# Kernel tuning notes

Hardware: AMD Instinct MI355X
Metric: run time of the kernel (lower is better)

Reference implementation:

```python
import jax, jax.numpy as jnp
import numpy as np

N_NODES = 40000
N_EDGES = 640000
N_GRAPHS = 64
F_IN = 32       # fourier_order*4
D_EMB = 256     # int(0.5*512)
D_HID = 512     # int(0.5*1024)
D_FC = 1024     # int(0.5*2048)
N_CLS = 10


def setup_inputs() -> dict:
    key = jax.random.key(0)
    ks = iter(jax.random.split(key, 40))
    rn = lambda shape, s=0.05: jax.random.normal(next(ks), shape, jnp.float32) * s
    inp = {
        'x': jax.random.normal(next(ks), (N_NODES, F_IN), jnp.float32),
        'edge_index': jax.random.randint(next(ks), (2, N_EDGES), 0, N_NODES, jnp.int32),
        'edge_attr': jax.random.uniform(next(ks), (N_EDGES, 1), jnp.float32),
        'batch': jnp.sort(jax.random.randint(next(ks), (N_NODES,), 0, N_GRAPHS, jnp.int32)),
        # embedding MLP
        'emb_w1': rn((F_IN, D_EMB)), 'emb_b1': jnp.zeros((D_EMB,), jnp.float32),
        'emb_w2': rn((D_EMB, D_EMB)), 'emb_b2': jnp.zeros((D_EMB,), jnp.float32),
        # edge_proj MLP
        'ep_w1': rn((1, 64)), 'ep_b1': jnp.zeros((64,), jnp.float32),
        'ep_w2': rn((64, 1)), 'ep_b2': jnp.zeros((1,), jnp.float32),
        # GCNConv weights (x @ W + b, PyG convention)
        'w_c1': rn((D_EMB, D_HID)), 'b_c1': jnp.zeros((D_HID,), jnp.float32),
        'w_c2': rn((D_HID, D_HID)), 'b_c2': jnp.zeros((D_HID,), jnp.float32),
        'w_c3': rn((D_HID, D_HID)), 'b_c3': jnp.zeros((D_HID,), jnp.float32),
        'w_c4': rn((D_HID, D_HID)), 'b_c4': jnp.zeros((D_HID,), jnp.float32),
        'w_c5': rn((D_HID, D_HID)), 'b_c5': jnp.zeros((D_HID,), jnp.float32),
        'w_c6': rn((D_HID, D_HID)), 'b_c6': jnp.zeros((D_HID,), jnp.float32),
        # head
        'fc1_w': rn((D_HID, D_FC)), 'fc1_b': jnp.zeros((D_FC,), jnp.float32),
        'head_w': rn((D_FC, N_CLS)), 'head_b': jnp.zeros((N_CLS,), jnp.float32),
    }
    return inp


def _gcn_conv(x, src, dst, norm, W, b):
    # PyG GCNConv: linear transform, then normalized scatter-add aggregation, then bias
    h = x @ W                                   # [N, d_out]
    msg = h[src] * norm[:, None]                # [E+N, d_out] gathered messages
    agg = jax.ops.segment_sum(msg, dst, num_segments=N_NODES)
    return agg + b


def _forward(x, edge_attr, emb_w1, emb_b1, emb_w2, emb_b2, ep_w1, ep_b1, ep_w2, ep_b2,
             w_c1, b_c1, w_c2, b_c2, w_c3, b_c3, w_c4, b_c4, w_c5, b_c5, w_c6, b_c6,
             fc1_w, fc1_b, head_w, head_b, edge_index, batch):
    # edge weights from edge_proj MLP (sigmoid output in (0,1))
    ew = jax.nn.sigmoid(jax.nn.relu(edge_attr @ ep_w1 + ep_b1) @ ep_w2 + ep_b2)[:, 0]  # [E]
    # gcn_norm with self loops (identical for every conv layer -> compute once)
    loops = jnp.arange(N_NODES, dtype=edge_index.dtype)
    src = jnp.concatenate([edge_index[0], loops])
    dst = jnp.concatenate([edge_index[1], loops])
    w = jnp.concatenate([ew, jnp.ones((N_NODES,), ew.dtype)])
    deg = jax.ops.segment_sum(w, dst, num_segments=N_NODES)
    dinv = jnp.where(deg > 0, jax.lax.rsqrt(jnp.maximum(deg, 1e-12)), 0.0)
    norm = dinv[src] * w * dinv[dst]            # [E+N]

    h = jax.nn.relu(jax.nn.relu(x @ emb_w1 + emb_b1) @ emb_w2 + emb_b2)
    h = _gcn_conv(h, src, dst, norm, w_c1, b_c1)
    skip = jax.nn.relu(h)
    h = _gcn_conv(skip, src, dst, norm, w_c2, b_c2)
    h = jax.nn.relu(h)
    h = _gcn_conv(h, src, dst, norm, w_c3, b_c3)
    skip = jax.nn.relu(h) + skip                # has_skip=True
    h = _gcn_conv(skip, src, dst, norm, w_c4, b_c4)  # is_deep=True
    h = jax.nn.relu(h)
    h = _gcn_conv(h, src, dst, norm, w_c5, b_c5)
    h = jax.nn.relu(h)
    h = _gcn_conv(h, src, dst, norm, w_c6, b_c6)
    skip = jax.nn.relu(h) + skip

    # global mean pool over graphs
    sums = jax.ops.segment_sum(skip, batch, num_segments=N_GRAPHS)
    cnts = jax.ops.segment_sum(jnp.ones((N_NODES,), skip.dtype), batch, num_segments=N_GRAPHS)
    pooled = sums / jnp.maximum(cnts, 1.0)[:, None]   # [G, D_HID]

    out = jax.nn.relu(pooled @ fc1_w + fc1_b) @ head_w + head_b   # [G, N_CLS]
    return out


def reference(x, edge_index, edge_attr, batch, emb_w1, emb_b1, emb_w2, emb_b2,
              ep_w1, ep_b1, ep_w2, ep_b2, w_c1, b_c1, w_c2, b_c2, w_c3, b_c3,
              w_c4, b_c4, w_c5, b_c5, w_c6, b_c6, fc1_w, fc1_b, head_w, head_b):
    return _forward(x, edge_attr, emb_w1, emb_b1, emb_w2, emb_b2, ep_w1, ep_b1, ep_w2, ep_b2,
                    w_c1, b_c1, w_c2, b_c2, w_c3, b_c3, w_c4, b_c4, w_c5, b_c5, w_c6, b_c6,
                    fc1_w, fc1_b, head_w, head_b, edge_index, batch)
```

## Files before the change

### kernel.cpp

```cpp
#include <hip/hip_runtime.h>
#include <math.h>

#define N_NODES 40000
#define MP      40192
#define NROWB   157
#define N_EDGES 640000
#define N_GRAPHS 64
#define F_IN 32
#define D_EMB 256
#define D_HID 512
#define D_FC 1024
#define N_CLS 10

typedef _Float16 f16x8 __attribute__((ext_vector_type(8)));
typedef float f32x4  __attribute__((ext_vector_type(4)));
typedef unsigned short u16;

template <int N> struct VecU;
template <> struct VecU<2> { typedef unsigned T __attribute__((ext_vector_type(2))); };
template <> struct VecU<4> { typedef unsigned T __attribute__((ext_vector_type(4))); };

__device__ __forceinline__ float h2f(u16 u) {
    union { u16 s; _Float16 h; } v; v.s = u; return (float)v.h;
}
__device__ __forceinline__ u16 f2h(float f) {
    union { u16 s; _Float16 h; } v; v.h = (_Float16)f; return v.s;
}
__device__ __forceinline__ void async16(void* lds, const void* g) {
    __builtin_amdgcn_global_load_lds((const __attribute__((address_space(1))) void*)g,
                                     (__attribute__((address_space(3))) void*)lds, 16, 0, 0);
}

__device__ __forceinline__ int pk_idx(int r, int q) {
    int rp = r >> 1;
    int g  = (((r & 1) << 2) | q) ^ (rp & 7);
    return rp * 64 + g * 8;
}

__global__ void prep_all(const float* __restrict__ x, u16* __restrict__ xb, u16* __restrict__ G,
                         float* __restrict__ deg, int* __restrict__ cnt, int* __restrict__ cursor,
                         float* __restrict__ sums) {
    int i = blockIdx.x * blockDim.x + threadIdx.x;
    if (i < N_NODES) { deg[i] = 1.0f; cnt[i] = 0; cursor[i] = 0; }
    if (i < MP * F_IN) {
        int row = i >> 5, colk = i & 31;
        float v = (row < N_NODES) ? x[i] : 0.f;
        size_t idx = (size_t)(row >> 8) * 8192 + pk_idx(row & 255, colk >> 3) + (colk & 7);
        xb[idx] = f2h(v);
    }
    if (i < 16 * 3072) {
        int kc = i / 3072, rem = i % 3072;
        G[(size_t)(156 * 16 + kc) * 8192 + 5120 + rem] = 0;
    } else if (i < 16 * 3072 + 8 * 3072) {
        int j = i - 16 * 3072;
        int kc = j / 3072, rem = j % 3072;
        G[(size_t)(156 * 8 + kc) * 8192 + 5120 + rem] = 0;
    }
    if (i < N_GRAPHS * D_HID) sums[i] = 0.f;
}

__global__ void edge_mlp_deg(const float* __restrict__ edge_attr,
                             const float* __restrict__ ep_w1, const float* __restrict__ ep_b1,
                             const float* __restrict__ ep_w2, const float* __restrict__ ep_b2,
                             const int* __restrict__ dst,
                             float* __restrict__ ew, float* __restrict__ deg, int* __restrict__ cnt) {
    __shared__ float w1[64], b1[64], w2[64];
    int t = threadIdx.x;
    if (t < 64) { w1[t] = ep_w1[t]; b1[t] = ep_b1[t]; w2[t] = ep_w2[t]; }
    __syncthreads();
    int e = blockIdx.x * blockDim.x + t;
    if (e >= N_EDGES) return;
    float x = edge_attr[e];
    float s = ep_b2[0];
#pragma unroll
    for (int j = 0; j < 64; ++j) s += fmaxf(x * w1[j] + b1[j], 0.f) * w2[j];
    float sig = 1.f / (1.f + expf(-s));
    ew[e] = sig;
    int d = dst[e];
    atomicAdd(&deg[d], sig);
    atomicAdd(&cnt[d], 1);
}

__global__ void dinv_kernel(const float* __restrict__ deg, float* __restrict__ dinv,
                            float* __restrict__ nloop) {
    int i = blockIdx.x * blockDim.x + threadIdx.x;
    if (i >= N_NODES) return;
    float d = deg[i];
    float r = (d > 0.f) ? rsqrtf(fmaxf(d, 1e-12f)) : 0.f;
    dinv[i] = r;
    nloop[i] = r * r;
}

__global__ void scan_kernel(const int* __restrict__ cnt, int* __restrict__ rowptr) {
    __shared__ int part[1024];
    int t = threadIdx.x;
    const int PER = (N_NODES + 1023) / 1024;
    int base = t * PER;
    int s = 0;
    for (int k = 0; k < PER; ++k) { int i = base + k; if (i < N_NODES) s += cnt[i]; }
    part[t] = s;
    __syncthreads();
    for (int off = 1; off < 1024; off <<= 1) {
        int v = (t >= off) ? part[t - off] : 0;
        __syncthreads();
        part[t] += v;
        __syncthreads();
    }
    int run = (t == 0) ? 0 : part[t - 1];
    for (int k = 0; k < PER; ++k) {
        int i = base + k;
        if (i < N_NODES) { rowptr[i] = run; run += cnt[i]; }
    }
    if (t == 1023) rowptr[N_NODES] = run;
}

__global__ void fill_csr_kernel(const int* __restrict__ src, const int* __restrict__ dst,
                                const float* __restrict__ ew, const float* __restrict__ dinv,
                                const int* __restrict__ rowptr, int* __restrict__ cursor,
                                int2* __restrict__ cv) {
    int e = blockIdx.x * blockDim.x + threadIdx.x;
    if (e >= N_EDGES) return;
    int d = dst[e];
    int s = src[e];
    float n = dinv[s] * ew[e] * dinv[d];
    int p = rowptr[d] + atomicAdd(&cursor[d], 1);
    cv[p] = make_int2(s, __float_as_int(n));
}

struct WPair { const float* s; u16* d; int K; int N; };
struct WP8 { WPair m[8]; };

__global__ void wprep_all(WP8 a) {
    __shared__ u16 th[32][33];
    WPair w = a.m[blockIdx.z];
    int n0 = blockIdx.x * 32;
    int k0 = blockIdx.y * 32;
    if (n0 >= w.N || k0 >= w.K) return;
    int tx = threadIdx.x, ty = threadIdx.y;
#pragma unroll
    for (int r = 0; r < 4; ++r) {
        int k = ty + r * 8;
        th[k][tx] = f2h(w.s[(size_t)(k0 + k) * w.N + n0 + tx]);
    }
    __syncthreads();
#pragma unroll
    for (int r = 0; r < 4; ++r) {
        int n = ty + r * 8;
        int R = n0 + n;
        int kcol = k0 + tx;
        size_t idx = ((size_t)(R >> 7) * (w.K >> 5) + (kcol >> 5)) * 4096
                   + pk_idx(R & 127, (kcol >> 3) & 3) + (kcol & 7);
        w.d[idx] = th[tx][n];
    }
}

__launch_bounds__(512)
__global__ void mfma_gemm(const u16* __restrict__ A,
                          const u16* __restrict__ W,
                          const float* __restrict__ bias,
                          const u16* __restrict__ skip,
                          u16* __restrict__ C, u16* __restrict__ Cpk,
                          int K, int N,
                          const int* __restrict__ batch, float* __restrict__ pool) {
    __shared__ __align__(16) u16 Wl[32768];
    __shared__ int sbatch[128];

    const int nColB = N >> 6;
    int b = blockIdx.x;
    int rowI = (b >> 3) / nColB * 8 + (b & 7);
    int colI = (b >> 3) % nColB;
    if (rowI >= NROWB) return;
    int rowBase = rowI * 256;
    int colBase = colI * 64;

    int t = threadIdx.x;
    int lane = t & 63;
    int wave = t >> 6;
    int quad = lane >> 4;
    int mrow = lane & 15;
    int nIter = K >> 5;

    int sw = (((mrow & 1) << 2) | quad) ^ ((mrow >> 1) & 7);
    int laneA = (wave * 16 + (mrow >> 1)) * 64 + sw * 8;
    int laneW = (mrow >> 1) * 64 + sw * 8;

    const u16* pA = A + (size_t)rowI * nIter * 8192;

    f16x8 aA0 = *(const f16x8*)&pA[laneA];
    f16x8 aA1 = *(const f16x8*)&pA[laneA + 512];
    f16x8 aB0, aB1;

    {
        const u16* ws = W + ((size_t)(colI >> 1) * nIter) * 4096 + (colI & 1) * 2048;
        for (int kc = wave; kc < nIter; kc += 8) {
            const u16* s = ws + (size_t)kc * 4096;
            u16* d = &Wl[kc * 2048];
            async16(&d[0],    s + lane * 8);
            async16(&d[512],  s + 512 + lane * 8);
            async16(&d[1024], s + 1024 + lane * 8);
            async16(&d[1536], s + 1536 + lane * 8);
        }
    }
    asm volatile("s_waitcnt vmcnt(0)" ::: "memory");
    __syncthreads();

    f32x4 acc[2][4] = {};

    for (int it = 0; it < nIter; it += 2) {
        if (it + 1 < nIter) {
            const u16* nA = pA + (size_t)(it + 1) * 8192;
            aB0 = *(const f16x8*)&nA[laneA];
            aB1 = *(const f16x8*)&nA[laneA + 512];
        }
        __builtin_amdgcn_sched_barrier(0);
        {
            const u16* Wc = &Wl[it * 2048];
#pragma unroll
            for (int j = 0; j < 4; ++j) {
                f16x8 w = *(const f16x8*)&Wc[laneW + j * 512];
                acc[0][j] = __builtin_amdgcn_mfma_f32_16x16x32_f16(aA0, w, acc[0][j], 0, 0, 0);
                acc[1][j] = __builtin_amdgcn_mfma_f32_16x16x32_f16(aA1, w, acc[1][j], 0, 0, 0);
            }
        }
        if (it + 1 < nIter) {
            if (it + 2 < nIter) {
                const u16* nA = pA + (size_t)(it + 2) * 8192;
                aA0 = *(const f16x8*)&nA[laneA];
                aA1 = *(const f16x8*)&nA[laneA + 512];
            }
            __builtin_amdgcn_sched_barrier(0);
            const u16* Wc = &Wl[(it + 1) * 2048];
#pragma unroll
            for (int j = 0; j < 4; ++j) {
                f16x8 w = *(const f16x8*)&Wc[laneW + j * 512];
                acc[0][j] = __builtin_amdgcn_mfma_f32_16x16x32_f16(aB0, w, acc[0][j], 0, 0, 0);
                acc[1][j] = __builtin_amdgcn_mfma_f32_16x16x32_f16(aB1, w, acc[1][j], 0, 0, 0);
            }
        }
    }
    __syncthreads();

    u16* eb = Wl;
    const int ES = 72;
#pragma unroll
    for (int ph = 0; ph < 2; ++ph) {
        if ((wave >> 2) == ph) {
#pragma unroll
            for (int j = 0; j < 4; ++j) {
                int col = colBase + j * 16 + mrow;
                float bv = bias[col];
#pragma unroll
                for (int i = 0; i < 2; ++i) {
#pragma unroll
                    for (int r = 0; r < 4; ++r) {
                        int lr = (wave & 3) * 32 + i * 16 + quad * 4 + r;
                        size_t row = (size_t)rowBase + ph * 128 + lr;
                        float v = fmaxf(acc[i][j][r] + bv, 0.f);
                        if (skip) v += h2f(skip[row * N + col]);
                        eb[lr * ES + j * 16 + mrow] = f2h(v);
                    }
                }
            }
        }
        if (pool && t < 128) {
            int row = rowBase + ph * 128 + t;
            sbatch[t] = (row < N_NODES) ? batch[row] : -1;
        }
        __syncthreads();
        if (C) {
#pragma unroll
            for (int k2 = 0; k2 < 2; ++k2) {
                int c = t + k2 * 512;
                int row = c >> 3, ch = c & 7;
                f16x8 v = *(const f16x8*)&eb[row * ES + ch * 8];
                *(f16x8*)&C[(size_t)(rowBase + ph * 128 + row) * N + colBase + ch * 8] = v;
            }
        } else if (Cpk) {
#pragma unroll
            for (int k2 = 0; k2 < 2; ++k2) {
                int c = t + k2 * 512;
                int row = c >> 3, ch = c & 7;
                f16x8 v = *(const f16x8*)&eb[row * ES + ch * 8];
                size_t idx = ((size_t)rowI * (N >> 5) + (colBase >> 5) + (ch >> 2)) * 8192
                           + pk_idx(ph * 128 + row, ch & 3);
                *(f16x8*)&Cpk[idx] = v;
            }
        }
        if (pool) {
            int c = t & 63;
            int rs = (t >> 6) * 16;
            float run = 0.f; int g = -1;
            for (int r = rs; r < rs + 16; ++r) {
                int bg = sbatch[r];
                if (bg != g) {
                    if (g >= 0) atomicAdd(&pool[(size_t)g * D_HID + colBase + c], run);
                    run = 0.f; g = bg;
                }
                if (bg >= 0) run += h2f(eb[r * ES + c]);
            }
            if (g >= 0) atomicAdd(&pool[(size_t)g * D_HID + colBase + c], run);
        }
        __syncthreads();
    }
}

template <int D>
__launch_bounds__(256)
__global__ void gather_f16(const u16* __restrict__ h, const int* __restrict__ rowptr,
                           const int2* __restrict__ cv, const float* __restrict__ nloop,
                           u16* __restrict__ out) {
    constexpr int FPL = D / 64;
    constexpr int UPL = FPL / 2;
    using VU = typename VecU<UPL>::T;
    int node = blockIdx.x * 4 + (threadIdx.x >> 6);
    int lane = threadIdx.x & 63;
    if (node >= N_NODES) return;
    union UU { unsigned u; _Float16 h[2]; };
    float acc[FPL];
    float sl = nloop[node];
    {
        VU own = *(const VU*)(h + (size_t)node * D + lane * FPL);
#pragma unroll
        for (int u = 0; u < UPL; ++u) {
            UU w; w.u = own[u];
            acc[2 * u]     = (float)w.h[0] * sl;
            acc[2 * u + 1] = (float)w.h[1] * sl;
        }
    }
    int beg = rowptr[node], end = rowptr[node + 1];
    if (end > beg) {
        int last = end - 1;
        int2 c[8];
#pragma unroll
        for (int m = 0; m < 8; ++m) c[m] = cv[min(beg + m, last)];
        for (int j = beg; j < end; j += 8) {
            VU tv[8];
#pragma unroll
            for (int m = 0; m < 8; ++m)
                tv[m] = *(const VU*)(h + (size_t)c[m].x * D + lane * FPL);
            int jn = j + 8;
            int2 cn[8];
#pragma unroll
            for (int m = 0; m < 8; ++m) cn[m] = c[m];
            if (jn < end) {
#pragma unroll
                for (int m = 0; m < 8; ++m) cn[m] = cv[min(jn + m, last)];
            }
            __builtin_amdgcn_sched_barrier(0);
#pragma unroll
            for (int m = 0; m < 8; ++m) {
                float v = (j + m < end) ? __int_as_float(c[m].y) : 0.f;
#pragma unroll
                for (int u = 0; u < UPL; ++u) {
                    UU w; w.u = tv[m][u];
                    acc[2 * u]     += (float)w.h[0] * v;
                    acc[2 * u + 1] += (float)w.h[1] * v;
                }
            }
#pragma unroll
            for (int m = 0; m < 8; ++m) c[m] = cn[m];
        }
    }
    VU o;
#pragma unroll
    for (int u = 0; u < UPL; ++u) {
        unsigned lo = f2h(acc[2 * u]);
        unsigned hi = f2h(acc[2 * u + 1]);
        o[u] = lo | (hi << 16);
    }
    size_t blkb = (size_t)(node >> 8) * (D >> 5);
    int rr = node & 255;
    if (D == 512) {
        size_t idx = (blkb + (lane >> 2)) * 8192 + pk_idx(rr, lane & 3);
        *(VU*)(out + idx) = o;
    } else {
        size_t idx = (blkb + (lane >> 3)) * 8192 + pk_idx(rr, (lane >> 1) & 3) + (lane & 1) * 4;
        *(VU*)(out + idx) = o;
    }
}

__launch_bounds__(1024)
__global__ void fc1_head(const float* __restrict__ sums, const int* __restrict__ batch,
                         const float* __restrict__ fc1_w, const float* __restrict__ fc1_b,
                         const float* __restrict__ head_w, const float* __restrict__ head_b,
                         float* __restrict__ out) {
    __shared__ float sv[D_HID];
    __shared__ float hacc[N_CLS];
    __shared__ float invc;
    int g = blockIdx.x;
    int t = threadIdx.x;
    if (t == 0) {
        int lo = 0, hi = N_NODES;
        while (lo < hi) { int m = (lo + hi) >> 1; if (batch[m] < g) lo = m + 1; else hi = m; }
        int lb = lo;
        lo = lb; hi = N_NODES;
        while (lo < hi) { int m = (lo + hi) >> 1; if (batch[m] < g + 1) lo = m + 1; else hi = m; }
        invc = 1.f / fmaxf((float)(lo - lb), 1.f);
    }
    if (t < N_CLS) hacc[t] = 0.f;
    __syncthreads();
    if (t < D_HID) sv[t] = sums[(size_t)g * D_HID + t] * invc;
    __syncthreads();
    int j = t;
    float acc = fc1_b[j];
#pragma unroll 8
    for (int k = 0; k < D_HID; ++k) acc += sv[k] * fc1_w[(size_t)k * D_FC + j];
    float f = fmaxf(acc, 0.f);
    float p[N_CLS];
#pragma unroll
    for (int c = 0; c < N_CLS; ++c) p[c] = f * head_w[j * N_CLS + c];
#pragma unroll
    for (int c = 0; c < N_CLS; ++c) {
        float v = p[c];
        for (int off = 32; off; off >>= 1) v += __shfl_down(v, off, 64);
        if ((t & 63) == 0) atomicAdd(&hacc[c], v);
    }
    __syncthreads();
    if (t < N_CLS) out[g * N_CLS + t] = hacc[t] + head_b[t];
}

extern "C" void kernel_launch(void* const* d_in, const int* in_sizes, int n_in,
                              void* d_out, int out_size, void* d_ws, size_t ws_size,
                              hipStream_t stream) {
    const float* x          = (const float*)d_in[0];
    const int*   edge_index = (const int*)d_in[1];
    const float* edge_attr  = (const float*)d_in[2];
    const int*   batch      = (const int*)d_in[3];
    const float* emb_w1 = (const float*)d_in[4];
    const float* emb_b1 = (const float*)d_in[5];
    const float* emb_w2 = (const float*)d_in[6];
    const float* emb_b2 = (const float*)d_in[7];
    const float* ep_w1  = (const float*)d_in[8];
    const float* ep_b1  = (const float*)d_in[9];
    const float* ep_w2  = (const float*)d_in[10];
    const float* ep_b2  = (const float*)d_in[11];
    const float* w_c[6] = { (const float*)d_in[12], (const float*)d_in[14], (const float*)d_in[16],
                            (const float*)d_in[18], (const float*)d_in[20], (const float*)d_in[22] };
    const float* b_c[6] = { (const float*)d_in[13], (const float*)d_in[15], (const float*)d_in[17],
                            (const float*)d_in[19], (const float*)d_in[21], (const float*)d_in[23] };
    const float* fc1_w  = (const float*)d_in[24];
    const float* fc1_b  = (const float*)d_in[25];
    const float* head_w = (const float*)d_in[26];
    const float* head_b = (const float*)d_in[27];
    float* out = (float*)d_out;

    const int* src = edge_index;
    const int* dst = edge_index + N_EDGES;

    char* p = (char*)d_ws;
    auto alloc = [&](size_t bytes) { char* r = p; p += (bytes + 255) & ~(size_t)255; return r; };
    float* ew    = (float*)alloc(N_EDGES * 4);
    float* deg   = (float*)alloc(N_NODES * 4);
    float* dinv  = (float*)alloc(N_NODES * 4);
    float* nloop = (float*)alloc(N_NODES * 4);
    int* cnt     = (int*)alloc(N_NODES * 4);
    int* cursor  = (int*)alloc(N_NODES * 4);
    int* rowptr  = (int*)alloc((N_NODES + 1) * 4);
    int2* cv     = (int2*)alloc((size_t)N_EDGES * 8);
    u16* xb = (u16*)alloc((size_t)MP * F_IN * 2);
    u16* H1 = (u16*)alloc((size_t)MP * D_EMB * 2);
    u16* H2 = (u16*)alloc((size_t)MP * D_EMB * 2);
    u16* G  = (u16*)alloc((size_t)MP * D_HID * 2);
    u16* S1 = (u16*)alloc((size_t)MP * D_HID * 2);
    u16* S2 = (u16*)alloc((size_t)MP * D_HID * 2);
    u16* Cb = (u16*)alloc((size_t)MP * D_HID * 2);
    u16* we1 = (u16*)alloc((size_t)F_IN * D_EMB * 2);
    u16* we2 = (u16*)alloc((size_t)D_EMB * D_EMB * 2);
    u16* wc[6];
    wc[0] = (u16*)alloc((size_t)D_EMB * D_HID * 2);
    for (int i = 1; i < 6; ++i) wc[i] = (u16*)alloc((size_t)D_HID * D_HID * 2);
    float* sums = (float*)alloc(N_GRAPHS * D_HID * 4);

    const int TB = 256;
    const int EB = (N_EDGES + TB - 1) / TB;
    const int NB = (N_NODES + TB - 1) / TB;

    prep_all<<<(MP * F_IN + TB - 1) / TB, TB, 0, stream>>>(x, xb, G, deg, cnt, cursor, sums);
    edge_mlp_deg<<<EB, TB, 0, stream>>>(edge_attr, ep_w1, ep_b1, ep_w2, ep_b2, dst, ew, deg, cnt);
    dinv_kernel<<<NB, TB, 0, stream>>>(deg, dinv, nloop);
    scan_kernel<<<1, 1024, 0, stream>>>(cnt, rowptr);
    fill_csr_kernel<<<EB, TB, 0, stream>>>(src, dst, ew, dinv, rowptr, cursor, cv);

    WP8 wp;
    wp.m[0] = { emb_w1, we1, F_IN,  D_EMB };
    wp.m[1] = { emb_w2, we2, D_EMB, D_EMB };
    wp.m[2] = { w_c[0], wc[0], D_EMB, D_HID };
    for (int i = 1; i < 6; ++i) wp.m[2 + i] = { w_c[i], wc[i], D_HID, D_HID };
    wprep_all<<<dim3(16, 16, 8), dim3(32, 8), 0, stream>>>(wp);

    const int SLOTS = ((NROWB + 7) / 8) * 8;
    const int GRID2 = SLOTS * (D_EMB / 64);
    const int GRID4 = SLOTS * (D_HID / 64);
    mfma_gemm<<<GRID2, 512, 0, stream>>>(xb, we1, emb_b1, nullptr, nullptr, H1, F_IN, D_EMB, nullptr, nullptr);
    mfma_gemm<<<GRID2, 512, 0, stream>>>(H1, we2, emb_b2, nullptr, H2, nullptr, D_EMB, D_EMB, nullptr, nullptr);

    const int GG = (N_NODES + 3) / 4;
    gather_f16<D_EMB><<<GG, 256, 0, stream>>>(H2, rowptr, cv, nloop, G);
    mfma_gemm<<<GRID4, 512, 0, stream>>>(G, wc[0], b_c[0], nullptr, S1, nullptr, D_EMB, D_HID, nullptr, nullptr);
    gather_f16<D_HID><<<GG, 256, 0, stream>>>(S1, rowptr, cv, nloop, G);
    mfma_gemm<<<GRID4, 512, 0, stream>>>(G, wc[1], b_c[1], nullptr, Cb, nullptr, D_HID, D_HID, nullptr, nullptr);
    gather_f16<D_HID><<<GG, 256, 0, stream>>>(Cb, rowptr, cv, nloop, G);
    mfma_gemm<<<GRID4, 512, 0, stream>>>(G, wc[2], b_c[2], S1, S2, nullptr, D_HID, D_HID, nullptr, nullptr);
    gather_f16<D_HID><<<GG, 256, 0, stream>>>(S2, rowptr, cv, nloop, G);
    mfma_gemm<<<GRID4, 512, 0, stream>>>(G, wc[3], b_c[3], nullptr, Cb, nullptr, D_HID, D_HID, nullptr, nullptr);
    gather_f16<D_HID><<<GG, 256, 0, stream>>>(Cb, rowptr, cv, nloop, G);
    mfma_gemm<<<GRID4, 512, 0, stream>>>(G, wc[4], b_c[4], nullptr, Cb, nullptr, D_HID, D_HID, nullptr, nullptr);
    gather_f16<D_HID><<<GG, 256, 0, stream>>>(Cb, rowptr, cv, nloop, G);
    mfma_gemm<<<GRID4, 512, 0, stream>>>(G, wc[5], b_c[5], S2, nullptr, nullptr, D_HID, D_HID, batch, sums);

    fc1_head<<<N_GRAPHS, 1024, 0, stream>>>(sums, batch, fc1_w, fc1_b, head_w, head_b, out);
}
```

Before: 1.132 ms.

## Split gather into column slices so each block covers many nodes on one slice

New measurement: 1.088 ms. 3.9% less time.

```diff
diff --git a/kernel.cpp b/kernel.cpp
--- a/kernel.cpp
+++ b/kernel.cpp
@@ -309,19 +309,25 @@
 __global__ void gather_f16(const u16* __restrict__ h, const int* __restrict__ rowptr,
                            const int2* __restrict__ cv, const float* __restrict__ nloop,
                            u16* __restrict__ out) {
-    constexpr int FPL = D / 64;
-    constexpr int UPL = FPL / 2;
-    using VU = typename VecU<UPL>::T;
-    int node = blockIdx.x * 4 + (threadIdx.x >> 6);
-    int lane = threadIdx.x & 63;
+    constexpr int COLS = D / 8;
+    constexpr int LPG  = COLS / 8;
+    constexpr int NPB  = 256 / LPG;
+    using VU = typename VecU<4>::T;
+    int b = blockIdx.x;
+    int slice = b & 7;
+    int ng = b >> 3;
+    int t = threadIdx.x;
+    int node = ng * NPB + t / LPG;
+    int l = t % LPG;
     if (node >= N_NODES) return;
+    const u16* hs = h + slice * COLS + l * 8;
     union UU { unsigned u; _Float16 h[2]; };
-    float acc[FPL];
+    float acc[8];
     float sl = nloop[node];
     {
-        VU own = *(const VU*)(h + (size_t)node * D + lane * FPL);
-#pragma unroll
-        for (int u = 0; u < UPL; ++u) {
+        VU own = *(const VU*)(hs + (size_t)node * D);
+#pragma unroll
+        for (int u = 0; u < 4; ++u) {
             UU w; w.u = own[u];
             acc[2 * u]     = (float)w.h[0] * sl;
             acc[2 * u + 1] = (float)w.h[1] * sl;
@@ -337,7 +343,7 @@
             VU tv[8];
 #pragma unroll
             for (int m = 0; m < 8; ++m)
-                tv[m] = *(const VU*)(h + (size_t)c[m].x * D + lane * FPL);
+                tv[m] = *(const VU*)(hs + (size_t)c[m].x * D);
             int jn = j + 8;
             int2 cn[8];
 #pragma unroll
@@ -351,7 +357,7 @@
             for (int m = 0; m < 8; ++m) {
                 float v = (j + m < end) ? __int_as_float(c[m].y) : 0.f;
 #pragma unroll
-                for (int u = 0; u < UPL; ++u) {
+                for (int u = 0; u < 4; ++u) {
                     UU w; w.u = tv[m][u];
                     acc[2 * u]     += (float)w.h[0] * v;
                     acc[2 * u + 1] += (float)w.h[1] * v;
@@ -363,20 +369,17 @@
     }
     VU o;
 #pragma unroll
-    for (int u = 0; u < UPL; ++u) {
+    for (int u = 0; u < 4; ++u) {
         unsigned lo = f2h(acc[2 * u]);
         unsigned hi = f2h(acc[2 * u + 1]);
         o[u] = lo | (hi << 16);
     }
     size_t blkb = (size_t)(node >> 8) * (D >> 5);
     int rr = node & 255;
-    if (D == 512) {
-        size_t idx = (blkb + (lane >> 2)) * 8192 + pk_idx(rr, lane & 3);
-        *(VU*)(out + idx) = o;
-    } else {
-        size_t idx = (blkb + (lane >> 3)) * 8192 + pk_idx(rr, (lane >> 1) & 3) + (lane & 1) * 4;
-        *(VU*)(out + idx) = o;
-    }
+    int kc, q;
+    if (D == 512) { kc = slice * 2 + (l >> 2); q = l & 3; }
+    else          { kc = slice;                q = l;     }
+    *(VU*)(out + (blkb + kc) * 8192 + pk_idx(rr, q)) = o;
 }
 
 __launch_bounds__(1024)
@@ -494,18 +497,19 @@
     mfma_gemm<<<GRID2, 512, 0, stream>>>(xb, we1, emb_b1, nullptr, nullptr, H1, F_IN, D_EMB, nullptr, nullptr);
     mfma_gemm<<<GRID2, 512, 0, stream>>>(H1, we2, emb_b2, nullptr, H2, nullptr, D_EMB, D_EMB, nullptr, nullptr);
 
-    const int GG = (N_NODES + 3) / 4;
-    gather_f16<D_EMB><<<GG, 256, 0, stream>>>(H2, rowptr, cv, nloop, G);
+    const int GG256 = (N_NODES / 64) * 8;
+    const int GG512 = (N_NODES / 32) * 8;
+    gather_f16<D_EMB><<<GG256, 256, 0, stream>>>(H2, rowptr, cv, nloop, G);
     mfma_gemm<<<GRID4, 512, 0, stream>>>(G, wc[0], b_c[0], nullptr, S1, nullptr, D_EMB, D_HID, nullptr, nullptr);
-    gather_f16<D_HID><<<GG, 256, 0, stream>>>(S1, rowptr, cv, nloop, G);
+    gather_f16<D_HID><<<GG512, 256, 0, stream>>>(S1, rowptr, cv, nloop, G);
     mfma_gemm<<<GRID4, 512, 0, stream>>>(G, wc[1], b_c[1], nullptr, Cb, nullptr, D_HID, D_HID, nullptr, nullptr);
-    gather_f16<D_HID><<<GG, 256, 0, stream>>>(Cb, rowptr, cv, nloop, G);
+    gather_f16<D_HID><<<GG512, 256, 0, stream>>>(Cb, rowptr, cv, nloop, G);
     mfma_gemm<<<GRID4, 512, 0, stream>>>(G, wc[2], b_c[2], S1, S2, nullptr, D_HID, D_HID, nullptr, nullptr);
-    gather_f16<D_HID><<<GG, 256, 0, stream>>>(S2, rowptr, cv, nloop, G);
+    gather_f16<D_HID><<<GG512, 256, 0, stream>>>(S2, rowptr, cv, nloop, G);
     mfma_gemm<<<GRID4, 512, 0, stream>>>(G, wc[3], b_c[3], nullptr, Cb, nullptr, D_HID, D_HID, nullptr, nullptr);
-    gather_f16<D_HID><<<GG, 256, 0, stream>>>(Cb, rowptr, cv, nloop, G);
+    gather_f16<D_HID><<<GG512, 256, 0, stream>>>(Cb, rowptr, cv, nloop, G);
     mfma_gemm<<<GRID4, 512, 0, stream>>>(G, wc[4], b_c[4], nullptr, Cb, nullptr, D_HID, D_HID, nullptr, nullptr);
-    gather_f16<D_HID><<<GG, 256, 0, stream>>>(Cb, rowptr, cv, nloop, G);
+    gather_f16<D_HID><<<GG512, 256, 0, stream>>>(Cb, rowptr, cv, nloop, G);
     mfma_gemm<<<GRID4, 512, 0, stream>>>(G, wc[5], b_c[5], S2, nullptr, nullptr, D_HID, D_HID, batch, sums);
 
     fc1_head<<<N_GRAPHS, 1024, 0, stream>>>(sums, batch, fc1_w, fc1_b, head_w, head_b, out);
```
